# Performance work log

Hardware: AMD Instinct MI355X
Metric: run time of the kernel (lower is better)

The kernel has to match this reference:

```python
import jax, jax.numpy as jnp
import numpy as np

N_HEADS = 8


def setup_inputs() -> dict:
    key = jax.random.key(0)
    ks = jax.random.split(key, 6)
    B, U, Lx, Ly = 16, 512, 1024, 1024
    x = jax.random.normal(ks[0], (B, U, Lx), dtype=jnp.float32)
    y = jax.random.normal(ks[1], (B, U, Ly), dtype=jnp.float32)
    xy_mask = jax.random.randint(ks[2], (B, Lx, Ly), 0, 2).astype(jnp.bool_)
    wq = jax.random.normal(ks[3], (U, U), dtype=jnp.float32) * (1.0 / np.sqrt(U))
    wk = jax.random.normal(ks[4], (U, U), dtype=jnp.float32) * (1.0 / np.sqrt(U))
    wo = jax.random.normal(ks[5], (U, U), dtype=jnp.float32) * (1.0 / np.sqrt(U))
    return {"x": x, "y": y, "xy_mask": xy_mask, "wq": wq, "wk": wk, "wo": wo}


def reference(x, y, xy_mask, wq, wk, wo):
    # x: (B, U, Lx), y: (B, U, Ly), xy_mask: (B, Lx, Ly)
    B, U, Lx = x.shape
    Ly = y.shape[2]
    H = N_HEADS
    d = U // H
    scale = 1.0 / (d ** 0.5)

    # 1x1 conv (bias=False) == channel-mixing matmul; weight layout (out, in)
    Q = jnp.einsum('ou,bul->bol', wq, x)   # (B, U, Lx)
    K = jnp.einsum('ou,bul->bol', wk, y)   # (B, U, Ly)

    # split channels into heads (head-major channel order, matching torch.split)
    Qh = Q.reshape(B, H, d, Lx)
    Kh = K.reshape(B, H, d, Ly)

    # ReLU-scored attention with mask (no softmax)
    A = jnp.einsum('bhdx,bhdy->bhxy', Qh, Kh)           # (B, H, Lx, Ly)
    A = jnp.maximum(A, 0.0) * scale
    A = jnp.where(xy_mask[:, None, :, :], A, 0.0)

    C = jnp.einsum('bhxy,bhdy->bhdx', A, Kh).reshape(B, U, Lx)

    # per-row element-count normalization (rows with zero count use 1)
    n_el = jnp.maximum(jnp.sum(xy_mask, axis=2), 1)     # (B, Lx)
    C = C / n_el[:, None, :].astype(x.dtype)

    E = 0.5 * (Q + C)
    return jnp.einsum('ou,bul->bol', wo, E)
```

## Files before the change

kernel.cpp:

```cpp
#include <hip/hip_runtime.h>
#include <stdint.h>
#include <stddef.h>

#define B_  16
#define U_  512
#define LX_ 1024
#define LY_ 1024
#define H_  8
#define D_  64

typedef unsigned short ushort_t;
typedef unsigned int   uint_t;
typedef __bf16 v8bf  __attribute__((ext_vector_type(8)));
typedef float  v16f  __attribute__((ext_vector_type(16)));

__device__ __forceinline__ ushort_t bf16u(float f) {
    uint_t u = __float_as_uint(f);
    uint_t r = (u + 0x7FFFu + ((u >> 16) & 1u)) >> 16;
    return (ushort_t)r;
}
__device__ __forceinline__ float bfu2f(ushort_t u) {
    return __uint_as_float(((uint_t)u) << 16);
}
__device__ __forceinline__ uint_t pkbf16(float f0, float f1) {
    uint_t u0 = __float_as_uint(f0), u1 = __float_as_uint(f1);
    u0 = u0 + 0x7FFFu + ((u0 >> 16) & 1u);
    u1 = u1 + 0x7FFFu + ((u1 >> 16) & 1u);
    return __builtin_amdgcn_perm(u1, u0, 0x07060302u);
}
__device__ __forceinline__ void gload16(const void* g, void* l) {
    auto gp = (const __attribute__((address_space(1))) uint32_t*)(uintptr_t)g;
    auto lp = (__attribute__((address_space(3))) uint32_t*)(uintptr_t)l;
    __builtin_amdgcn_global_load_lds(gp, lp, 16, 0, 0);
}

__global__ void detect_kernel(const uint_t* __restrict__ mask, int* __restrict__ flag) {
    __shared__ int s;
    if (threadIdx.x == 0) s = 0;
    __syncthreads();
    int c = 0;
    for (int i = threadIdx.x; i < 1024; i += 256) c += (mask[i] <= 1u) ? 1 : 0;
    atomicAdd(&s, c);
    __syncthreads();
    if (threadIdx.x == 0) *flag = (s >= 1000) ? 1 : 0;
}

__global__ __launch_bounds__(256) void nelmask_kernel(const void* __restrict__ mask,
                                                      const int* __restrict__ flag,
                                                      float* __restrict__ nel,
                                                      uint_t* __restrict__ mb) {
    int row  = blockIdx.x * 4 + (threadIdx.x >> 6);
    int lane = threadIdx.x & 63;
    const int isInt = *flag;
    const uint8_t* m8  = (const uint8_t*)mask + (size_t)row * LY_;
    const int*     m32 = (const int*)mask + (size_t)row * LY_;
    int cnt = 0;
    for (int yg = 0; yg < LY_ / 64; ++yg) {
        int y = yg * 64 + lane;
        bool p = isInt ? (m32[y] != 0) : (m8[y] != 0);
        unsigned long long bal = __ballot(p);
        if (lane == 0) {
            mb[(size_t)row * 32 + yg * 2]     = (uint_t)bal;
            mb[(size_t)row * 32 + yg * 2 + 1] = (uint_t)(bal >> 32);
            cnt += __popcll(bal);
        }
    }
    if (lane == 0) nel[row] = (float)(cnt > 0 ? cnt : 1);
}

__global__ __launch_bounds__(256) void castw_kernel(const float* __restrict__ w0,
                                                    const float* __restrict__ w1,
                                                    const float* __restrict__ w2,
                                                    ushort_t* __restrict__ o0,
                                                    ushort_t* __restrict__ o1,
                                                    ushort_t* __restrict__ o2) {
    const float* s = blockIdx.y == 0 ? w0 : (blockIdx.y == 1 ? w1 : w2);
    ushort_t*    d = blockIdx.y == 0 ? o0 : (blockIdx.y == 1 ? o1 : o2);
    int i = (blockIdx.x * 256 + threadIdx.x) * 4;
    float4 v = *(const float4*)&s[i];
    ushort4 p;
    p.x = bf16u(v.x); p.y = bf16u(v.y); p.z = bf16u(v.z); p.w = bf16u(v.w);
    *(ushort4*)&d[i] = p;
}

__global__ __launch_bounds__(256) void castT_kernel(const float* __restrict__ X,
                                                    const float* __restrict__ Y,
                                                    ushort_t* __restrict__ XT,
                                                    ushort_t* __restrict__ YT) {
    const int l0 = blockIdx.x * 64;
    const int u0 = blockIdx.y * 64;
    const int b  = blockIdx.z & 15;
    const int sel = blockIdx.z >> 4;
    const float* S = sel ? Y : X;
    ushort_t*  Dst = sel ? YT : XT;
    __shared__ ushort_t T[64][72];
    const int tid = threadIdx.x;
    #pragma unroll
    for (int e = 0; e < 4; ++e) {
        int ci = e * 256 + tid;
        int r = ci >> 4, c4 = (ci & 15) * 4;
        float4 v = *(const float4*)&S[((size_t)(b * U_ + u0 + r) << 10) + l0 + c4];
        T[r][c4 + 0] = bf16u(v.x); T[r][c4 + 1] = bf16u(v.y);
        T[r][c4 + 2] = bf16u(v.z); T[r][c4 + 3] = bf16u(v.w);
    }
    __syncthreads();
    #pragma unroll
    for (int e = 0; e < 2; ++e) {
        int ci = e * 256 + tid;
        int lr = ci >> 3, cc = ci & 7;
        ushort_t tmp[8];
        #pragma unroll
        for (int j = 0; j < 8; ++j) tmp[j] = T[cc * 8 + j][lr];
        *(uint4*)&Dst[((size_t)((b << 10) + l0 + lr)) * U_ + u0 + cc * 8] = *(uint4*)tmp;
    }
}

template <int OUTF32>
__global__ __launch_bounds__(256) void gemm_mfma(const ushort_t* __restrict__ A, size_t aStr,
                                                 const ushort_t* __restrict__ Bm, size_t bStr,
                                                 void* __restrict__ Out, size_t oStr, int ldOut) {
    const int n0 = blockIdx.x * 128;
    const int m0 = blockIdx.y * 128;
    const int b  = blockIdx.z;
    __shared__ __align__(16) ushort_t As[128 * 64];
    __shared__ __align__(16) ushort_t Bs[128 * 64];
    const int tid = threadIdx.x;
    const ushort_t* Ab = A + aStr * b;
    const ushort_t* Bb = Bm + bStr * b;

    const int w = tid >> 6, lane = tid & 63, lo = lane & 31, hi = lane >> 5;
    const int wm = (w >> 1) * 64, wn = (w & 1) * 64;

    v16f acc00, acc01, acc10, acc11;
    #pragma unroll
    for (int i = 0; i < 16; ++i) { acc00[i] = 0.f; acc01[i] = 0.f; acc10[i] = 0.f; acc11[i] = 0.f; }

    for (int kk = 0; kk < 8; ++kk) {
        const int k0 = kk * 64;
        #pragma unroll
        for (int e = 0; e < 4; ++e) {
            int ci = e * 256 + tid;
            int r = ci >> 3, c = ci & 7;
            int g = (c ^ (r & 7)) << 3;
            gload16(&Ab[(size_t)(m0 + r) * U_ + k0 + g], &As[ci * 8]);
            gload16(&Bb[(size_t)(n0 + r) * U_ + k0 + g], &Bs[ci * 8]);
        }
        __syncthreads();
        #pragma unroll
        for (int ks = 0; ks < 4; ++ks) {
            int ch = ks * 2 + hi;
            int rA0 = wm + lo, rA1 = wm + 32 + lo;
            int rB0 = wn + lo, rB1 = wn + 32 + lo;
            v8bf a0 = *(v8bf*)&As[rA0 * 64 + ((ch ^ (rA0 & 7)) << 3)];
            v8bf a1 = *(v8bf*)&As[rA1 * 64 + ((ch ^ (rA1 & 7)) << 3)];
            v8bf b0 = *(v8bf*)&Bs[rB0 * 64 + ((ch ^ (rB0 & 7)) << 3)];
            v8bf b1 = *(v8bf*)&Bs[rB1 * 64 + ((ch ^ (rB1 & 7)) << 3)];
            acc00 = __builtin_amdgcn_mfma_f32_32x32x16_bf16(a0, b0, acc00, 0, 0, 0);
            acc01 = __builtin_amdgcn_mfma_f32_32x32x16_bf16(a0, b1, acc01, 0, 0, 0);
            acc10 = __builtin_amdgcn_mfma_f32_32x32x16_bf16(a1, b0, acc10, 0, 0, 0);
            acc11 = __builtin_amdgcn_mfma_f32_32x32x16_bf16(a1, b1, acc11, 0, 0, 0);
        }
        __syncthreads();
    }

    #pragma unroll
    for (int mi = 0; mi < 2; ++mi) {
        #pragma unroll
        for (int nj = 0; nj < 2; ++nj) {
            v16f c = mi ? (nj ? acc11 : acc10) : (nj ? acc01 : acc00);
            int n = n0 + wn + nj * 32 + lo;
            #pragma unroll
            for (int r = 0; r < 16; ++r) {
                int m = m0 + wm + mi * 32 + (r & 3) + 8 * (r >> 2) + 4 * hi;
                size_t addr = oStr * b + (size_t)m * ldOut + n;
                if (OUTF32) ((float*)Out)[addr] = c[r];
                else        ((ushort_t*)Out)[addr] = bf16u(c[r]);
            }
        }
    }
}

__global__ __launch_bounds__(256) void ktranspose_kernel(const ushort_t* __restrict__ Ka,
                                                         ushort_t* __restrict__ Kb) {
    const int y0 = blockIdx.x * 64;
    const int h  = blockIdx.y;
    const int b  = blockIdx.z;
    __shared__ ushort_t T[64][72];
    const int tid = threadIdx.x;

    #pragma unroll
    for (int e = 0; e < 2; ++e) {
        int idx = e * 256 + tid;
        int d = idx >> 3, c = idx & 7;
        uint4 v = *(const uint4*)&Ka[((size_t)(b * U_ + h * D_ + d) << 10) + y0 + c * 8];
        *(uint4*)&T[d][c * 8] = v;
    }
    __syncthreads();
    #pragma unroll
    for (int e = 0; e < 2; ++e) {
        int idx = e * 256 + tid;
        int yy = idx >> 3, dc = idx & 7;
        ushort_t tmp[8];
        #pragma unroll
        for (int j = 0; j < 8; ++j) tmp[j] = T[dc * 8 + j][yy];
        *(uint4*)&Kb[(((size_t)(b * H_ + h) << 10) + y0 + yy) * D_ + dc * 8] = *(uint4*)tmp;
    }
}

typedef uint_t v2u __attribute__((ext_vector_type(2)));

__device__ __forceinline__ void conv_sblock(const v16f& s, uint_t wbh, v8bf* fr) {
    uint_t pk[8];
    #pragma unroll
    for (int i = 0; i < 8; ++i) {
        float f0 = fmaxf(s[2 * i + 0], 0.f);
        float f1 = fmaxf(s[2 * i + 1], 0.f);
        uint_t r;
        asm("v_cvt_pk_bf16_f32 %0, %1, %2" : "=v"(r) : "v"(f0), "v"(f1));
        pk[i] = r;
    }
    #pragma unroll
    for (int t = 0; t < 2; ++t) {
        auto ra = __builtin_amdgcn_permlane32_swap(pk[4 * t + 0], pk[4 * t + 2], false, false);
        auto rb = __builtin_amdgcn_permlane32_swap(pk[4 * t + 1], pk[4 * t + 3], false, false);
        uint_t w0 = ra[0];
        uint_t w1 = rb[0];
        uint_t w2 = ra[1];
        uint_t w3 = rb[1];
        uint_t u0 = wbh >> (t * 16 + 0);
        uint_t u1 = wbh >> (t * 16 + 2);
        uint_t u2 = wbh >> (t * 16 + 4);
        uint_t u3 = wbh >> (t * 16 + 6);
        w0 &= ((u0 & 1u) * 0xFFFFu) | ((u0 & 2u) * 0x7FFF8000u);
        w1 &= ((u1 & 1u) * 0xFFFFu) | ((u1 & 2u) * 0x7FFF8000u);
        w2 &= ((u2 & 1u) * 0xFFFFu) | ((u2 & 2u) * 0x7FFF8000u);
        w3 &= ((u3 & 1u) * 0xFFFFu) | ((u3 & 2u) * 0x7FFF8000u);
        union { uint_t u[4]; v8bf b; } cv;
        cv.u[0] = w0; cv.u[1] = w1; cv.u[2] = w2; cv.u[3] = w3;
        fr[t] = cv.b;
    }
}

__global__ __launch_bounds__(256, 4) void attn_mfma(const ushort_t* __restrict__ QTg,
                                                    const ushort_t* __restrict__ Ka_g,
                                                    const ushort_t* __restrict__ Kb_g,
                                                    const uint_t* __restrict__ mbits,
                                                    const float* __restrict__ nel,
                                                    ushort_t* __restrict__ ETg) {
    const int tid = threadIdx.x;
    const int id  = blockIdx.x;
    const int bh  = id & 127;
    const int x0g = (id >> 7) * 128;
    const int b = bh >> 3, h = bh & 7;

    __shared__ __align__(16) ushort_t SM[4 * 4096];

    const int w    = tid >> 6;
    const int lane = tid & 63;
    const int lo   = lane & 31;
    const int hi   = lane >> 5;
    const int xq   = w * 32;

    const ushort_t* KaBase = Ka_g + ((size_t)(b * U_ + h * D_)) * LY_;
    const ushort_t* KbBase = Kb_g + ((size_t)(b * H_ + h)) * LY_ * D_;
    const int bx = b * LX_ + x0g;
    const int xg = bx + xq + lo;

    #pragma unroll
    for (int e = 0; e < 2; ++e) {
        int ci = e * 256 + tid;
        int r = ci >> 3, c = ci & 7;
        int g8 = (c ^ (r & 7)) << 3;
        gload16(&KbBase[(size_t)r * D_ + g8], &SM[ci * 8]);
        gload16(&KaBase[(size_t)r * LY_ + g8], &SM[8192 + ci * 8]);
    }

    v8bf qf[4];
    {
        const ushort_t* q0 = QTg + (size_t)xg * U_ + h * D_;
        #pragma unroll
        for (int kt = 0; kt < 4; ++kt) qf[kt] = *(const v8bf*)&q0[(kt * 2 + hi) * 8];
    }

    v16f acc0, acc1;
    #pragma unroll
    for (int i = 0; i < 16; ++i) { acc0[i] = 0.f; acc1[i] = 0.f; }

    __syncthreads();

    for (int tt = 0; tt < 16; ++tt) {
        ushort_t* KBc = SM + (tt & 1) * 4096;
        ushort_t* KAc = SM + 8192 + (tt & 1) * 4096;

        if (tt < 15) {
            ushort_t* KBn = SM + ((tt + 1) & 1) * 4096;
            ushort_t* KAn = SM + 8192 + ((tt + 1) & 1) * 4096;
            const int yn = tt * 64 + 64;
            #pragma unroll
            for (int e = 0; e < 2; ++e) {
                int ci = e * 256 + tid;
                int r = ci >> 3, c = ci & 7;
                int g8 = (c ^ (r & 7)) << 3;
                gload16(&KbBase[(size_t)(yn + r) * D_ + g8], &KBn[ci * 8]);
                gload16(&KaBase[(size_t)r * LY_ + yn + g8], &KAn[ci * 8]);
            }
        }
        v2u wb = *(const v2u*)&mbits[(size_t)xg * 32 + tt * 2];

        v8bf fr0[2], fr1[2];
        {
            v16f s;
            #pragma unroll
            for (int i = 0; i < 16; ++i) s[i] = 0.f;
            #pragma unroll
            for (int kt = 0; kt < 4; ++kt) {
                int ch = kt * 2 + hi;
                v8bf a = *(v8bf*)&KBc[lo * 64 + ((ch ^ (lo & 7)) << 3)];
                s = __builtin_amdgcn_mfma_f32_32x32x16_bf16(a, qf[kt], s, 0, 0, 0);
            }
            conv_sblock(s, wb[0] >> (hi * 8), fr0);
        }
        {
            v16f s;
            #pragma unroll
            for (int i = 0; i < 16; ++i) s[i] = 0.f;
            #pragma unroll
            for (int kt = 0; kt < 4; ++kt) {
                int ch = kt * 2 + hi;
                v8bf a = *(v8bf*)&KBc[(32 + lo) * 64 + ((ch ^ ((32 + lo) & 7)) << 3)];
                s = __builtin_amdgcn_mfma_f32_32x32x16_bf16(a, qf[kt], s, 0, 0, 0);
            }
            conv_sblock(s, wb[1] >> (hi * 8), fr1);
        }

        #pragma unroll
        for (int kt = 0; kt < 4; ++kt) {
            int ch = kt * 2 + hi;
            v8bf frk = (kt < 2) ? fr0[kt] : fr1[kt - 2];
            v8bf a0 = *(v8bf*)&KAc[lo * 64 + ((ch ^ (lo & 7)) << 3)];
            v8bf a1 = *(v8bf*)&KAc[(32 + lo) * 64 + ((ch ^ ((32 + lo) & 7)) << 3)];
            acc0 = __builtin_amdgcn_mfma_f32_32x32x16_bf16(a0, frk, acc0, 0, 0, 0);
            acc1 = __builtin_amdgcn_mfma_f32_32x32x16_bf16(a1, frk, acc1, 0, 0, 0);
        }
        __syncthreads();
    }

    {
        ushort_t* Et = SM;
        const int xl = xq + lo;
        float invn = 0.0625f / nel[xg];
        const ushort_t* qg = QTg + (size_t)xg * U_ + h * D_ + 4 * hi;
        #pragma unroll
        for (int half = 0; half < 2; ++half) {
            const v16f& c = half ? acc1 : acc0;
            #pragma unroll
            for (int q = 0; q < 4; ++q) {
                int d0 = half * 32 + q * 8 + 4 * hi;
                ushort_t q4[4];
                *(uint2*)q4 = *(const uint2*)&qg[half * 32 + q * 8];
                ushort_t e4[4];
                e4[0] = bf16u(0.5f * bfu2f(q4[0]) + c[q * 4 + 0] * invn);
                e4[1] = bf16u(0.5f * bfu2f(q4[1]) + c[q * 4 + 1] * invn);
                e4[2] = bf16u(0.5f * bfu2f(q4[2]) + c[q * 4 + 2] * invn);
                e4[3] = bf16u(0.5f * bfu2f(q4[3]) + c[q * 4 + 3] * invn);
                int base = xl * 64 + ((((d0 >> 3) ^ (xl & 7)) << 3) | (4 * hi));
                *(uint2*)&Et[base] = *(uint2*)e4;
            }
        }
    }
    __syncthreads();
    #pragma unroll
    for (int e = 0; e < 4; ++e) {
        int idx = e * 256 + tid;
        int row = idx >> 3, cc = idx & 7;
        uint4 v = *(const uint4*)&SM[row * 64 + ((cc ^ (row & 7)) << 3)];
        *(uint4*)&ETg[((size_t)(bx + row)) * U_ + h * D_ + cc * 8] = v;
    }
}

extern "C" void kernel_launch(void* const* d_in, const int* in_sizes, int n_in,
                              void* d_out, int out_size, void* d_ws, size_t ws_size,
                              hipStream_t stream) {
    const float* x    = (const float*)d_in[0];
    const float* y    = (const float*)d_in[1];
    const void*  mask = d_in[2];
    const float* wq   = (const float*)d_in[3];
    const float* wk   = (const float*)d_in[4];
    const float* wo   = (const float*)d_in[5];

    char* wsb = (char*)d_ws;
    ushort_t* xT    = (ushort_t*)(wsb);
    ushort_t* yT    = (ushort_t*)(wsb + 16777216);
    ushort_t* Ka    = (ushort_t*)(wsb + 33554432);
    ushort_t* wqb   = (ushort_t*)(wsb + 50331648);
    ushort_t* wkb   = (ushort_t*)(wsb + 50855936);
    ushort_t* wob   = (ushort_t*)(wsb + 51380224);
    uint_t*   mbits = (uint_t*)(wsb + 51904512);
    float*    nel   = (float*)(wsb + 54001664);
    int*      flag  = (int*)(wsb + 54067200);
    ushort_t* ET    = xT;
    ushort_t* Kb    = yT;
    ushort_t* QT    = (ushort_t*)d_out;

    detect_kernel<<<1, 256, 0, stream>>>((const uint_t*)mask, flag);
    nelmask_kernel<<<(B_ * LX_) / 4, 256, 0, stream>>>(mask, flag, nel, mbits);
    castw_kernel<<<dim3(U_ * U_ / 1024, 3), 256, 0, stream>>>(wq, wk, wo, wqb, wkb, wob);
    castT_kernel<<<dim3(16, 8, 32), 256, 0, stream>>>(x, y, xT, yT);

    gemm_mfma<0><<<dim3(4, 8, B_), 256, 0, stream>>>(
        xT, (size_t)LX_ * U_, wqb, 0, (void*)QT, (size_t)LX_ * U_, U_);
    gemm_mfma<0><<<dim3(8, 4, B_), 256, 0, stream>>>(
        wkb, 0, yT, (size_t)LY_ * U_, (void*)Ka, (size_t)U_ * LY_, LY_);
    ktranspose_kernel<<<dim3(LY_ / 64, H_, B_), 256, 0, stream>>>(Ka, Kb);
    attn_mfma<<<1024, 256, 0, stream>>>(QT, Ka, Kb, mbits, nel, ET);
    gemm_mfma<1><<<dim3(8, 4, B_), 256, 0, stream>>>(
        wob, 0, ET, (size_t)LX_ * U_, d_out, (size_t)U_ * LX_, LX_);
}
```

Baseline: 283.9 us.

## Merge prep kernels, fuse Q/K GEMMs and fold K transpose into epilogue

The four preprocessing launches (mask type detection, mask bitpacking, weight casts, input transpose-casts) become one block-partitioned kernel, with mask detection repeated per mask block. The Q and K projection GEMMs run in a single launch, and the K GEMM epilogue writes the transposed per-head K layout directly, so the separate transpose kernel is gone. This cuts launch overhead and lets the two GEMMs fill the GPU together. In exchange the Kb writes from the epilogue are scattered 2-byte stores, Kb now lives in the upper half of the output buffer, and the mask-detection reads are duplicated in every mask block.

```diff
diff --git a/kernel.cpp b/kernel.cpp
--- a/kernel.cpp
+++ b/kernel.cpp
@@ -22,96 +22,172 @@
 __device__ __forceinline__ float bfu2f(ushort_t u) {
     return __uint_as_float(((uint_t)u) << 16);
 }
-__device__ __forceinline__ uint_t pkbf16(float f0, float f1) {
-    uint_t u0 = __float_as_uint(f0), u1 = __float_as_uint(f1);
-    u0 = u0 + 0x7FFFu + ((u0 >> 16) & 1u);
-    u1 = u1 + 0x7FFFu + ((u1 >> 16) & 1u);
-    return __builtin_amdgcn_perm(u1, u0, 0x07060302u);
-}
 __device__ __forceinline__ void gload16(const void* g, void* l) {
     auto gp = (const __attribute__((address_space(1))) uint32_t*)(uintptr_t)g;
     auto lp = (__attribute__((address_space(3))) uint32_t*)(uintptr_t)l;
     __builtin_amdgcn_global_load_lds(gp, lp, 16, 0, 0);
 }
 
-__global__ void detect_kernel(const uint_t* __restrict__ mask, int* __restrict__ flag) {
+__global__ __launch_bounds__(256) void prep_kernel(const float* __restrict__ X,
+                                                   const float* __restrict__ Y,
+                                                   const void* __restrict__ mask,
+                                                   const float* __restrict__ wq,
+                                                   const float* __restrict__ wk,
+                                                   const float* __restrict__ wo,
+                                                   ushort_t* __restrict__ XT,
+                                                   ushort_t* __restrict__ YT,
+                                                   ushort_t* __restrict__ wqb,
+                                                   ushort_t* __restrict__ wkb,
+                                                   ushort_t* __restrict__ wob,
+                                                   float* __restrict__ nel,
+                                                   uint_t* __restrict__ mb) {
+    __shared__ ushort_t T[64][72];
     __shared__ int s;
-    if (threadIdx.x == 0) s = 0;
-    __syncthreads();
-    int c = 0;
-    for (int i = threadIdx.x; i < 1024; i += 256) c += (mask[i] <= 1u) ? 1 : 0;
-    atomicAdd(&s, c);
-    __syncthreads();
-    if (threadIdx.x == 0) *flag = (s >= 1000) ? 1 : 0;
-}
-
-__global__ __launch_bounds__(256) void nelmask_kernel(const void* __restrict__ mask,
-                                                      const int* __restrict__ flag,
-                                                      float* __restrict__ nel,
-                                                      uint_t* __restrict__ mb) {
-    int row  = blockIdx.x * 4 + (threadIdx.x >> 6);
-    int lane = threadIdx.x & 63;
-    const int isInt = *flag;
-    const uint8_t* m8  = (const uint8_t*)mask + (size_t)row * LY_;
-    const int*     m32 = (const int*)mask + (size_t)row * LY_;
-    int cnt = 0;
-    for (int yg = 0; yg < LY_ / 64; ++yg) {
-        int y = yg * 64 + lane;
-        bool p = isInt ? (m32[y] != 0) : (m8[y] != 0);
-        unsigned long long bal = __ballot(p);
-        if (lane == 0) {
-            mb[(size_t)row * 32 + yg * 2]     = (uint_t)bal;
-            mb[(size_t)row * 32 + yg * 2 + 1] = (uint_t)(bal >> 32);
-            cnt += __popcll(bal);
-        }
-    }
-    if (lane == 0) nel[row] = (float)(cnt > 0 ? cnt : 1);
-}
-
-__global__ __launch_bounds__(256) void castw_kernel(const float* __restrict__ w0,
-                                                    const float* __restrict__ w1,
-                                                    const float* __restrict__ w2,
-                                                    ushort_t* __restrict__ o0,
-                                                    ushort_t* __restrict__ o1,
-                                                    ushort_t* __restrict__ o2) {
-    const float* s = blockIdx.y == 0 ? w0 : (blockIdx.y == 1 ? w1 : w2);
-    ushort_t*    d = blockIdx.y == 0 ? o0 : (blockIdx.y == 1 ? o1 : o2);
-    int i = (blockIdx.x * 256 + threadIdx.x) * 4;
-    float4 v = *(const float4*)&s[i];
-    ushort4 p;
-    p.x = bf16u(v.x); p.y = bf16u(v.y); p.z = bf16u(v.z); p.w = bf16u(v.w);
-    *(ushort4*)&d[i] = p;
-}
-
-__global__ __launch_bounds__(256) void castT_kernel(const float* __restrict__ X,
-                                                    const float* __restrict__ Y,
-                                                    ushort_t* __restrict__ XT,
-                                                    ushort_t* __restrict__ YT) {
-    const int l0 = blockIdx.x * 64;
-    const int u0 = blockIdx.y * 64;
-    const int b  = blockIdx.z & 15;
-    const int sel = blockIdx.z >> 4;
-    const float* S = sel ? Y : X;
-    ushort_t*  Dst = sel ? YT : XT;
-    __shared__ ushort_t T[64][72];
     const int tid = threadIdx.x;
-    #pragma unroll
-    for (int e = 0; e < 4; ++e) {
-        int ci = e * 256 + tid;
-        int r = ci >> 4, c4 = (ci & 15) * 4;
-        float4 v = *(const float4*)&S[((size_t)(b * U_ + u0 + r) << 10) + l0 + c4];
-        T[r][c4 + 0] = bf16u(v.x); T[r][c4 + 1] = bf16u(v.y);
-        T[r][c4 + 2] = bf16u(v.z); T[r][c4 + 3] = bf16u(v.w);
-    }
-    __syncthreads();
-    #pragma unroll
-    for (int e = 0; e < 2; ++e) {
-        int ci = e * 256 + tid;
-        int lr = ci >> 3, cc = ci & 7;
-        ushort_t tmp[8];
-        #pragma unroll
-        for (int j = 0; j < 8; ++j) tmp[j] = T[cc * 8 + j][lr];
-        *(uint4*)&Dst[((size_t)((b << 10) + l0 + lr)) * U_ + u0 + cc * 8] = *(uint4*)tmp;
+    const int bid = blockIdx.x;
+
+    if (bid < 4096) {
+        const int l0 = (bid & 15) * 64;
+        const int u0 = ((bid >> 4) & 7) * 64;
+        const int z  = bid >> 7;
+        const int b  = z & 15;
+        const int sel = z >> 4;
+        const float* S = sel ? Y : X;
+        ushort_t*  Dst = sel ? YT : XT;
+        #pragma unroll
+        for (int e = 0; e < 4; ++e) {
+            int ci = e * 256 + tid;
+            int r = ci >> 4, c4 = (ci & 15) * 4;
+            float4 v = *(const float4*)&S[((size_t)(b * U_ + u0 + r) << 10) + l0 + c4];
+            T[r][c4 + 0] = bf16u(v.x); T[r][c4 + 1] = bf16u(v.y);
+            T[r][c4 + 2] = bf16u(v.z); T[r][c4 + 3] = bf16u(v.w);
+        }
+        __syncthreads();
+        #pragma unroll
+        for (int e = 0; e < 2; ++e) {
+            int ci = e * 256 + tid;
+            int lr = ci >> 3, cc = ci & 7;
+            ushort_t tmp[8];
+            #pragma unroll
+            for (int j = 0; j < 8; ++j) tmp[j] = T[cc * 8 + j][lr];
+            *(uint4*)&Dst[((size_t)((b << 10) + l0 + lr)) * U_ + u0 + cc * 8] = *(uint4*)tmp;
+        }
+    } else if (bid < 8192) {
+        const uint_t* mw = (const uint_t*)mask;
+        if (tid == 0) s = 0;
+        __syncthreads();
+        int c = 0;
+        for (int i = tid; i < 1024; i += 256) c += (mw[i] <= 1u) ? 1 : 0;
+        atomicAdd(&s, c);
+        __syncthreads();
+        const int isInt = (s >= 1000) ? 1 : 0;
+
+        int row  = (bid - 4096) * 4 + (tid >> 6);
+        int lane = tid & 63;
+        const uint8_t* m8  = (const uint8_t*)mask + (size_t)row * LY_;
+        const int*     m32 = (const int*)mask + (size_t)row * LY_;
+        int cnt = 0;
+        for (int yg = 0; yg < LY_ / 64; ++yg) {
+            int yy = yg * 64 + lane;
+            bool p = isInt ? (m32[yy] != 0) : (m8[yy] != 0);
+            unsigned long long bal = __ballot(p);
+            if (lane == 0) {
+                mb[(size_t)row * 32 + yg * 2]     = (uint_t)bal;
+                mb[(size_t)row * 32 + yg * 2 + 1] = (uint_t)(bal >> 32);
+                cnt += __popcll(bal);
+            }
+        }
+        if (lane == 0) nel[row] = (float)(cnt > 0 ? cnt : 1);
+    } else {
+        int cb = bid - 8192;
+        int selw = cb >> 8;
+        const float* sw = selw == 0 ? wq : (selw == 1 ? wk : wo);
+        ushort_t*    dw = selw == 0 ? wqb : (selw == 1 ? wkb : wob);
+        int i = ((cb & 255) * 256 + tid) * 4;
+        float4 v = *(const float4*)&sw[i];
+        ushort4 p;
+        p.x = bf16u(v.x); p.y = bf16u(v.y); p.z = bf16u(v.z); p.w = bf16u(v.w);
+        *(ushort4*)&dw[i] = p;
+    }
+}
+
+__global__ __launch_bounds__(256) void gemm_qk(const ushort_t* __restrict__ xT,
+                                               const ushort_t* __restrict__ wqb,
+                                               const ushort_t* __restrict__ wkb,
+                                               const ushort_t* __restrict__ yT,
+                                               ushort_t* __restrict__ QT,
+                                               ushort_t* __restrict__ Ka,
+                                               ushort_t* __restrict__ Kb) {
+    __shared__ __align__(16) ushort_t As[128 * 64];
+    __shared__ __align__(16) ushort_t Bs[128 * 64];
+    const int tid = threadIdx.x;
+    const int id  = blockIdx.x;
+    const int isK = id >> 9;
+    const int lid = id & 511;
+    const int b   = lid >> 5;
+    int m0, n0, ldOut;
+    const ushort_t *Ab, *Bb;
+    ushort_t* Ob;
+    if (!isK) {
+        n0 = (lid & 3) * 128; m0 = ((lid >> 2) & 7) * 128;
+        Ab = xT + (size_t)b * (LX_ * U_); Bb = wqb;
+        Ob = QT + (size_t)b * (LX_ * U_); ldOut = U_;
+    } else {
+        n0 = (lid & 7) * 128; m0 = ((lid >> 3) & 3) * 128;
+        Ab = wkb; Bb = yT + (size_t)b * (LY_ * U_);
+        Ob = Ka + (size_t)b * (U_ * LY_); ldOut = LY_;
+    }
+
+    const int w = tid >> 6, lane = tid & 63, lo = lane & 31, hi = lane >> 5;
+    const int wm = (w >> 1) * 64, wn = (w & 1) * 64;
+
+    v16f acc00, acc01, acc10, acc11;
+    #pragma unroll
+    for (int i = 0; i < 16; ++i) { acc00[i] = 0.f; acc01[i] = 0.f; acc10[i] = 0.f; acc11[i] = 0.f; }
+
+    for (int kk = 0; kk < 8; ++kk) {
+        const int k0 = kk * 64;
+        #pragma unroll
+        for (int e = 0; e < 4; ++e) {
+            int ci = e * 256 + tid;
+            int r = ci >> 3, c = ci & 7;
+            int g = (c ^ (r & 7)) << 3;
+            gload16(&Ab[(size_t)(m0 + r) * U_ + k0 + g], &As[ci * 8]);
+            gload16(&Bb[(size_t)(n0 + r) * U_ + k0 + g], &Bs[ci * 8]);
+        }
+        __syncthreads();
+        #pragma unroll
+        for (int ks = 0; ks < 4; ++ks) {
+            int ch = ks * 2 + hi;
+            int rA0 = wm + lo, rA1 = wm + 32 + lo;
+            int rB0 = wn + lo, rB1 = wn + 32 + lo;
+            v8bf a0 = *(v8bf*)&As[rA0 * 64 + ((ch ^ (rA0 & 7)) << 3)];
+            v8bf a1 = *(v8bf*)&As[rA1 * 64 + ((ch ^ (rA1 & 7)) << 3)];
+            v8bf b0 = *(v8bf*)&Bs[rB0 * 64 + ((ch ^ (rB0 & 7)) << 3)];
+            v8bf b1 = *(v8bf*)&Bs[rB1 * 64 + ((ch ^ (rB1 & 7)) << 3)];
+            acc00 = __builtin_amdgcn_mfma_f32_32x32x16_bf16(a0, b0, acc00, 0, 0, 0);
+            acc01 = __builtin_amdgcn_mfma_f32_32x32x16_bf16(a0, b1, acc01, 0, 0, 0);
+            acc10 = __builtin_amdgcn_mfma_f32_32x32x16_bf16(a1, b0, acc10, 0, 0, 0);
+            acc11 = __builtin_amdgcn_mfma_f32_32x32x16_bf16(a1, b1, acc11, 0, 0, 0);
+        }
+        __syncthreads();
+    }
+
+    #pragma unroll
+    for (int mi = 0; mi < 2; ++mi) {
+        #pragma unroll
+        for (int nj = 0; nj < 2; ++nj) {
+            v16f c = mi ? (nj ? acc11 : acc10) : (nj ? acc01 : acc00);
+            int n = n0 + wn + nj * 32 + lo;
+            #pragma unroll
+            for (int r = 0; r < 16; ++r) {
+                int m = m0 + wm + mi * 32 + (r & 3) + 8 * (r >> 2) + 4 * hi;
+                ushort_t v = bf16u(c[r]);
+                Ob[(size_t)m * ldOut + n] = v;
+                if (isK)
+                    Kb[(((size_t)(b * H_ + (m >> 6)) << 10) + n) * D_ + (m & 63)] = v;
+            }
+        }
     }
 }
 
@@ -177,33 +253,6 @@
                 else        ((ushort_t*)Out)[addr] = bf16u(c[r]);
             }
         }
-    }
-}
-
-__global__ __launch_bounds__(256) void ktranspose_kernel(const ushort_t* __restrict__ Ka,
-                                                         ushort_t* __restrict__ Kb) {
-    const int y0 = blockIdx.x * 64;
-    const int h  = blockIdx.y;
-    const int b  = blockIdx.z;
-    __shared__ ushort_t T[64][72];
-    const int tid = threadIdx.x;
-
-    #pragma unroll
-    for (int e = 0; e < 2; ++e) {
-        int idx = e * 256 + tid;
-        int d = idx >> 3, c = idx & 7;
-        uint4 v = *(const uint4*)&Ka[((size_t)(b * U_ + h * D_ + d) << 10) + y0 + c * 8];
-        *(uint4*)&T[d][c * 8] = v;
-    }
-    __syncthreads();
-    #pragma unroll
-    for (int e = 0; e < 2; ++e) {
-        int idx = e * 256 + tid;
-        int yy = idx >> 3, dc = idx & 7;
-        ushort_t tmp[8];
-        #pragma unroll
-        for (int j = 0; j < 8; ++j) tmp[j] = T[dc * 8 + j][yy];
-        *(uint4*)&Kb[(((size_t)(b * H_ + h) << 10) + y0 + yy) * D_ + dc * 8] = *(uint4*)tmp;
     }
 }
 
@@ -397,21 +446,13 @@
     ushort_t* wob   = (ushort_t*)(wsb + 51380224);
     uint_t*   mbits = (uint_t*)(wsb + 51904512);
     float*    nel   = (float*)(wsb + 54001664);
-    int*      flag  = (int*)(wsb + 54067200);
     ushort_t* ET    = xT;
-    ushort_t* Kb    = yT;
     ushort_t* QT    = (ushort_t*)d_out;
-
-    detect_kernel<<<1, 256, 0, stream>>>((const uint_t*)mask, flag);
-    nelmask_kernel<<<(B_ * LX_) / 4, 256, 0, stream>>>(mask, flag, nel, mbits);
-    castw_kernel<<<dim3(U_ * U_ / 1024, 3), 256, 0, stream>>>(wq, wk, wo, wqb, wkb, wob);
-    castT_kernel<<<dim3(16, 8, 32), 256, 0, stream>>>(x, y, xT, yT);
-
-    gemm_mfma<0><<<dim3(4, 8, B_), 256, 0, stream>>>(
-        xT, (size_t)LX_ * U_, wqb, 0, (void*)QT, (size_t)LX_ * U_, U_);
-    gemm_mfma<0><<<dim3(8, 4, B_), 256, 0, stream>>>(
-        wkb, 0, yT, (size_t)LY_ * U_, (void*)Ka, (size_t)U_ * LY_, LY_);
-    ktranspose_kernel<<<dim3(LY_ / 64, H_, B_), 256, 0, stream>>>(Ka, Kb);
+    ushort_t* Kb    = (ushort_t*)d_out + (size_t)B_ * LX_ * U_;
+
+    prep_kernel<<<8960, 256, 0, stream>>>(x, y, mask, wq, wk, wo,
+                                          xT, yT, wqb, wkb, wob, nel, mbits);
+    gemm_qk<<<1024, 256, 0, stream>>>(xT, wqb, wkb, yT, QT, Ka, Kb);
     attn_mfma<<<1024, 256, 0, stream>>>(QT, Ka, Kb, mbits, nel, ET);
     gemm_mfma<1><<<dim3(8, 4, B_), 256, 0, stream>>>(
         wob, 0, ET, (size_t)LX_ * U_, d_out, (size_t)U_ * LX_, LX_);
```

Result: no change. 288.4 us (+1.6%).
